# Kernel tuning notes

Measured on AMD Instinct MI355X. Metric: run time of the kernel, lower is better.

Reference implementation:

```python
import jax, jax.numpy as jnp
import numpy as np

B, T, D, E = 8, 4096, 128, 16
TOP_K = 2


def setup_inputs() -> dict:
    key = jax.random.key(0)
    k1, k2, k3 = jax.random.split(key, 3)
    x = jax.random.normal(k1, (B, T, D), dtype=jnp.float32)
    Wg = jax.random.normal(k2, (D, E), dtype=jnp.float32) * 0.08   # gate Dense kernel
    bg = jnp.zeros((E,), dtype=jnp.float32)                         # gate Dense bias
    Ew = jax.random.normal(k3, (E, D, D), dtype=jnp.float32) * (1.0 / np.sqrt(D))  # expert weights
    return {"x": x, "Wg": Wg, "bg": bg, "Ew": Ew}


def reference(x, Wg, bg, Ew):
    # gate: Dense(n_experts, softmax) on x (context defaults to x)
    gate_scores = jax.nn.softmax(x @ Wg + bg, axis=-1)              # (B,T,E)
    top_vals, top_idx = jax.lax.top_k(gate_scores, TOP_K)           # (B,T,2)
    top_w = top_vals / (jnp.sum(top_vals, axis=-1, keepdims=True) + 1e-6)
    # all-expert transform (faithful to original dense einsum)
    expert_outputs = jnp.einsum('btd,edo->bteo', x, Ew)             # (B,T,E,D)
    # combine top-k one-hot masks with normalized weights -> per-expert weight
    onehot = jax.nn.one_hot(top_idx, E, dtype=x.dtype)              # (B,T,2,E)
    mask = jnp.sum(onehot * top_w[..., None], axis=2)               # (B,T,E)
    m = mask[..., None]                                             # (B,T,E,1)
    weighted_avg = jnp.sum(expert_outputs * m, axis=2)              # (B,T,D)
    diff_sq = jnp.square(expert_outputs - weighted_avg[:, :, None, :])
    weighted_var = jnp.sum(diff_sq * m, axis=2)                     # (B,T,D)
    consensus = jnp.exp(-jnp.mean(weighted_var, axis=-1))           # (B,T)
    return (weighted_avg, consensus)
```

## Files before the change

kernel.cpp:

```cpp
#include <hip/hip_runtime.h>
#include <hip/hip_bf16.h>

#define NTOK 32768
#define DD 128
#define NE 16
#define CSTRIDE 32

#define OFF_COUNTS 0
#define OFF_TOKW   (4*1024)
#define OFF_LISTS  (512*1024)
#define OFF_YBUF   (4*1024*1024)

__global__ __launch_bounds__(128) void gate_kernel(
    const float* __restrict__ x, const float* __restrict__ Wg,
    const float* __restrict__ bg,
    int* __restrict__ counts, int* __restrict__ lists, float* __restrict__ tokw)
{
    __shared__ float sWg[DD * NE];
    __shared__ int   sCnt[NE];
    __shared__ int   sBase[NE];
    const int tid = threadIdx.x;
    for (int i = tid; i < DD * NE; i += 128) sWg[i] = Wg[i];
    if (tid < NE) sCnt[tid] = 0;
    __syncthreads();

    const int t = blockIdx.x * 128 + tid;
    const float* xt = x + (size_t)t * DD;

    float logits[NE];
    #pragma unroll
    for (int e = 0; e < NE; ++e) logits[e] = bg[e];

    #pragma unroll 4
    for (int d4 = 0; d4 < DD / 4; ++d4) {
        float4 xv = ((const float4*)xt)[d4];
        float xs0 = xv.x, xs1 = xv.y, xs2 = xv.z, xs3 = xv.w;
        const float* w0 = &sWg[(d4 * 4 + 0) * NE];
        const float* w1 = &sWg[(d4 * 4 + 1) * NE];
        const float* w2 = &sWg[(d4 * 4 + 2) * NE];
        const float* w3 = &sWg[(d4 * 4 + 3) * NE];
        #pragma unroll
        for (int e = 0; e < NE; ++e) {
            float acc = logits[e];
            acc = fmaf(xs0, w0[e], acc);
            acc = fmaf(xs1, w1[e], acc);
            acc = fmaf(xs2, w2[e], acc);
            acc = fmaf(xs3, w3[e], acc);
            logits[e] = acc;
        }
    }

    float m = logits[0];
    #pragma unroll
    for (int e = 1; e < NE; ++e) m = fmaxf(m, logits[e]);
    float Z = 0.0f;
    #pragma unroll
    for (int e = 0; e < NE; ++e) Z += expf(logits[e] - m);

    int i1 = 0; float l1 = logits[0];
    #pragma unroll
    for (int e = 1; e < NE; ++e) if (logits[e] > l1) { l1 = logits[e]; i1 = e; }
    int i2 = -1; float l2 = -3.4e38f;
    #pragma unroll
    for (int e = 0; e < NE; ++e) if (e != i1 && logits[e] > l2) { l2 = logits[e]; i2 = e; }

    float p1 = expf(l1 - m) / Z;
    float p2 = expf(l2 - m) / Z;
    float s  = p1 + p2 + 1e-6f;
    tokw[t * 2 + 0] = p1 / s;
    tokw[t * 2 + 1] = p2 / s;

    int s1 = atomicAdd(&sCnt[i1], 1);
    int s2 = atomicAdd(&sCnt[i2], 1);
    __syncthreads();
    if (tid < NE) sBase[tid] = atomicAdd(&counts[tid * CSTRIDE], sCnt[tid]);
    __syncthreads();
    lists[i1 * NTOK + sBase[i1] + s1] = t * 2 + 0;
    lists[i2 * NTOK + sBase[i2] + s2] = t * 2 + 1;
}

__global__ __launch_bounds__(256) void expert_kernel(
    const float* __restrict__ x, const float* __restrict__ Ew,
    const int* __restrict__ counts, const int* __restrict__ lists,
    float* __restrict__ ybuf)
{
    const int e = blockIdx.y;
    const int count = counts[e * CSTRIDE];
    const int start = blockIdx.x * 64;
    if (start >= count) return;

    __shared__ int   sEnt[64];
    __shared__ float xs[DD][64];
    __shared__ float ews[32][DD];

    const int tid = threadIdx.x;
    if (tid < 64) {
        int idx = start + tid;
        sEnt[tid] = (idx < count) ? lists[e * NTOK + idx] : -1;
    }
    __syncthreads();

    for (int i = tid; i < 64 * 32; i += 256) {
        int tok = i & 63, d4 = i >> 6;
        int en = sEnt[tok];
        if (en >= 0) {
            float4 v = ((const float4*)(x + (size_t)(en >> 1) * DD))[d4];
            xs[d4 * 4 + 0][tok] = v.x;
            xs[d4 * 4 + 1][tok] = v.y;
            xs[d4 * 4 + 2][tok] = v.z;
            xs[d4 * 4 + 3][tok] = v.w;
        }
    }

    const int lane = tid & 63, wv = tid >> 6;
    const int o4 = lane & 15, tq = lane >> 4;
    const int tokb = wv * 16 + tq * 4;
    const int colb = o4 * 4;

    float acc[4][8];
    #pragma unroll
    for (int a = 0; a < 4; ++a)
        #pragma unroll
        for (int b = 0; b < 8; ++b) acc[a][b] = 0.0f;

    const float* EwE = Ew + (size_t)e * DD * DD;

    for (int kt = 0; kt < 4; ++kt) {
        __syncthreads();
        for (int i = tid; i < 32 * 32; i += 256) {
            int row = i >> 5, c4 = i & 31;
            ((float4*)&ews[row][0])[c4] =
                ((const float4*)(EwE + (size_t)(kt * 32 + row) * DD))[c4];
        }
        __syncthreads();

        #pragma unroll 4
        for (int d = 0; d < 32; ++d) {
            float4 xv = *(const float4*)&xs[kt * 32 + d][tokb];
            float4 e0 = *(const float4*)&ews[d][colb];
            float4 e1 = *(const float4*)&ews[d][colb + 64];
            float xt0 = xv.x, xt1 = xv.y, xt2 = xv.z, xt3 = xv.w;
            acc[0][0] = fmaf(xt0, e0.x, acc[0][0]); acc[0][1] = fmaf(xt0, e0.y, acc[0][1]);
            acc[0][2] = fmaf(xt0, e0.z, acc[0][2]); acc[0][3] = fmaf(xt0, e0.w, acc[0][3]);
            acc[0][4] = fmaf(xt0, e1.x, acc[0][4]); acc[0][5] = fmaf(xt0, e1.y, acc[0][5]);
            acc[0][6] = fmaf(xt0, e1.z, acc[0][6]); acc[0][7] = fmaf(xt0, e1.w, acc[0][7]);
            acc[1][0] = fmaf(xt1, e0.x, acc[1][0]); acc[1][1] = fmaf(xt1, e0.y, acc[1][1]);
            acc[1][2] = fmaf(xt1, e0.z, acc[1][2]); acc[1][3] = fmaf(xt1, e0.w, acc[1][3]);
            acc[1][4] = fmaf(xt1, e1.x, acc[1][4]); acc[1][5] = fmaf(xt1, e1.y, acc[1][5]);
            acc[1][6] = fmaf(xt1, e1.z, acc[1][6]); acc[1][7] = fmaf(xt1, e1.w, acc[1][7]);
            acc[2][0] = fmaf(xt2, e0.x, acc[2][0]); acc[2][1] = fmaf(xt2, e0.y, acc[2][1]);
            acc[2][2] = fmaf(xt2, e0.z, acc[2][2]); acc[2][3] = fmaf(xt2, e0.w, acc[2][3]);
            acc[2][4] = fmaf(xt2, e1.x, acc[2][4]); acc[2][5] = fmaf(xt2, e1.y, acc[2][5]);
            acc[2][6] = fmaf(xt2, e1.z, acc[2][6]); acc[2][7] = fmaf(xt2, e1.w, acc[2][7]);
            acc[3][0] = fmaf(xt3, e0.x, acc[3][0]); acc[3][1] = fmaf(xt3, e0.y, acc[3][1]);
            acc[3][2] = fmaf(xt3, e0.z, acc[3][2]); acc[3][3] = fmaf(xt3, e0.w, acc[3][3]);
            acc[3][4] = fmaf(xt3, e1.x, acc[3][4]); acc[3][5] = fmaf(xt3, e1.y, acc[3][5]);
            acc[3][6] = fmaf(xt3, e1.z, acc[3][6]); acc[3][7] = fmaf(xt3, e1.w, acc[3][7]);
        }
    }

    #pragma unroll
    for (int tt = 0; tt < 4; ++tt) {
        int en = sEnt[tokb + tt];
        if (en >= 0) {
            float* yr = ybuf + (size_t)en * DD;
            float4 a; a.x = acc[tt][0]; a.y = acc[tt][1]; a.z = acc[tt][2]; a.w = acc[tt][3];
            float4 b; b.x = acc[tt][4]; b.y = acc[tt][5]; b.z = acc[tt][6]; b.w = acc[tt][7];
            *(float4*)(yr + colb)      = a;
            *(float4*)(yr + colb + 64) = b;
        }
    }
}

__global__ __launch_bounds__(256) void combine_kernel(
    const float* __restrict__ ybuf, const float* __restrict__ tokw,
    float* __restrict__ avg_out, float* __restrict__ cons_out)
{
    const int tid = threadIdx.x;
    const int lane = tid & 63, wv = tid >> 6;
    const int t = blockIdx.x * 4 + wv;

    const float w1 = tokw[t * 2 + 0];
    const float w2 = tokw[t * 2 + 1];
    const float2 y1 = ((const float2*)(ybuf + (size_t)(t * 2 + 0) * DD))[lane];
    const float2 y2 = ((const float2*)(ybuf + (size_t)(t * 2 + 1) * DD))[lane];

    float a0 = w1 * y1.x + w2 * y2.x;
    float a1 = w1 * y1.y + w2 * y2.y;
    float2 av; av.x = a0; av.y = a1;
    ((float2*)(avg_out + (size_t)t * DD))[lane] = av;

    float d10 = y1.x - a0, d11 = y1.y - a1;
    float d20 = y2.x - a0, d21 = y2.y - a1;
    float v = w1 * (d10 * d10 + d11 * d11) + w2 * (d20 * d20 + d21 * d21);
    #pragma unroll
    for (int off = 32; off > 0; off >>= 1) v += __shfl_xor(v, off);
    if (lane == 0) cons_out[t] = expf(-v * (1.0f / 128.0f));
}

extern "C" void kernel_launch(void* const* d_in, const int* in_sizes, int n_in,
                              void* d_out, int out_size, void* d_ws, size_t ws_size,
                              hipStream_t stream)
{
    const float* x  = (const float*)d_in[0];
    const float* Wg = (const float*)d_in[1];
    const float* bg = (const float*)d_in[2];
    const float* Ew = (const float*)d_in[3];
    float* out = (float*)d_out;

    char* ws = (char*)d_ws;
    int*   counts = (int*)(ws + OFF_COUNTS);
    float* tokw   = (float*)(ws + OFF_TOKW);
    int*   lists  = (int*)(ws + OFF_LISTS);
    float* ybuf   = (float*)(ws + OFF_YBUF);

    hipMemsetAsync(counts, 0, NE * CSTRIDE * sizeof(int), stream);

    gate_kernel<<<NTOK / 128, 128, 0, stream>>>(x, Wg, bg, counts, lists, tokw);
    expert_kernel<<<dim3(NTOK / 64, NE), 256, 0, stream>>>(x, Ew, counts, lists, ybuf);
    combine_kernel<<<NTOK / 4, 256, 0, stream>>>(ybuf, tokw, out, out + (size_t)NTOK * DD);
}
```

Baseline: 134.2 us.

## Use bf16 MFMA for expert matmul with pre-transposed bf16 weights and activations

Replaces the fp32 scalar-FMA expert GEMM with bf16 16x16x32 MFMA instructions. A new kernel converts expert weights to a transposed bf16 layout, and the gate kernel now also writes a bf16 copy of x. The gate splits each token's dot product across 4 lanes joined by shuffles. The expert output buffer is stored in bf16, halving the traffic into the combine kernel, which now handles 4 tokens per wave. Precision drops to bf16 for inputs and intermediates, which risks accuracy against the fp32 reference. The extra conversion kernel and the added xb write add some work in exchange.

After: 125.0 us. 1.07x faster.

```diff
diff --git a/kernel.cpp b/kernel.cpp
--- a/kernel.cpp
+++ b/kernel.cpp
@@ -9,45 +9,95 @@
 #define OFF_COUNTS 0
 #define OFF_TOKW   (4*1024)
 #define OFF_LISTS  (512*1024)
-#define OFF_YBUF   (4*1024*1024)
-
-__global__ __launch_bounds__(128) void gate_kernel(
+#define OFF_XB     (3*1024*1024)
+#define OFF_EWT    (11*1024*1024)
+#define OFF_YBUF   (12*1024*1024)
+
+typedef __attribute__((ext_vector_type(8))) short bf16x8;
+typedef __attribute__((ext_vector_type(4))) float f32x4;
+
+static __device__ inline ushort f2bf(float f) {
+    uint u = __builtin_bit_cast(uint, f);
+    u = u + 0x7FFFu + ((u >> 16) & 1u);
+    return (ushort)(u >> 16);
+}
+static __device__ inline float b2f(ushort h) {
+    uint u = ((uint)h) << 16;
+    return __builtin_bit_cast(float, u);
+}
+
+__global__ __launch_bounds__(256) void ewt_kernel(
+    const float* __restrict__ Ew, ushort* __restrict__ ewT)
+{
+    __shared__ float tile[32][33];
+    const int b = blockIdx.x;
+    const int e = b >> 4, ki = ((b >> 2) & 3) * 32, oi = (b & 3) * 32;
+    const int tid = threadIdx.x;
+    const int r = tid >> 3, c4 = (tid & 7) * 4;
+    const float4 v = *(const float4*)(Ew + (size_t)e * DD * DD + (ki + r) * DD + oi + c4);
+    tile[r][c4 + 0] = v.x; tile[r][c4 + 1] = v.y;
+    tile[r][c4 + 2] = v.z; tile[r][c4 + 3] = v.w;
+    __syncthreads();
+    const int o = tid >> 3, k4 = (tid & 7) * 4;
+    ushort4 s;
+    s.x = f2bf(tile[k4 + 0][o]);
+    s.y = f2bf(tile[k4 + 1][o]);
+    s.z = f2bf(tile[k4 + 2][o]);
+    s.w = f2bf(tile[k4 + 3][o]);
+    *(ushort4*)(ewT + (size_t)e * DD * DD + (oi + o) * DD + ki + k4) = s;
+}
+
+__global__ __launch_bounds__(256) void gate_kernel(
     const float* __restrict__ x, const float* __restrict__ Wg,
     const float* __restrict__ bg,
-    int* __restrict__ counts, int* __restrict__ lists, float* __restrict__ tokw)
+    int* __restrict__ counts, int* __restrict__ lists, float* __restrict__ tokw,
+    ushort* __restrict__ xb)
 {
     __shared__ float sWg[DD * NE];
+    __shared__ float sBg[NE];
     __shared__ int   sCnt[NE];
     __shared__ int   sBase[NE];
     const int tid = threadIdx.x;
-    for (int i = tid; i < DD * NE; i += 128) sWg[i] = Wg[i];
-    if (tid < NE) sCnt[tid] = 0;
-    __syncthreads();
-
-    const int t = blockIdx.x * 128 + tid;
+    for (int i = tid; i < DD * NE; i += 256) sWg[i] = Wg[i];
+    if (tid < NE) { sBg[tid] = bg[tid]; sCnt[tid] = 0; }
+    __syncthreads();
+
+    const int t = blockIdx.x * 64 + (tid >> 2);
+    const int g = tid & 3;
     const float* xt = x + (size_t)t * DD;
+    ushort*      xo = xb + (size_t)t * DD;
 
     float logits[NE];
     #pragma unroll
-    for (int e = 0; e < NE; ++e) logits[e] = bg[e];
-
-    #pragma unroll 4
-    for (int d4 = 0; d4 < DD / 4; ++d4) {
-        float4 xv = ((const float4*)xt)[d4];
-        float xs0 = xv.x, xs1 = xv.y, xs2 = xv.z, xs3 = xv.w;
-        const float* w0 = &sWg[(d4 * 4 + 0) * NE];
-        const float* w1 = &sWg[(d4 * 4 + 1) * NE];
-        const float* w2 = &sWg[(d4 * 4 + 2) * NE];
-        const float* w3 = &sWg[(d4 * 4 + 3) * NE];
+    for (int e = 0; e < NE; ++e) logits[e] = 0.0f;
+
+    #pragma unroll
+    for (int i = 0; i < 8; ++i) {
+        const int d0 = g * 4 + i * 16;
+        float4 v = ((const float4*)xt)[g + i * 4];
+        const float* w0 = &sWg[(d0 + 0) * NE];
+        const float* w1 = &sWg[(d0 + 1) * NE];
+        const float* w2 = &sWg[(d0 + 2) * NE];
+        const float* w3 = &sWg[(d0 + 3) * NE];
         #pragma unroll
         for (int e = 0; e < NE; ++e) {
-            float acc = logits[e];
-            acc = fmaf(xs0, w0[e], acc);
-            acc = fmaf(xs1, w1[e], acc);
-            acc = fmaf(xs2, w2[e], acc);
-            acc = fmaf(xs3, w3[e], acc);
-            logits[e] = acc;
-        }
+            float a = logits[e];
+            a = fmaf(v.x, w0[e], a);
+            a = fmaf(v.y, w1[e], a);
+            a = fmaf(v.z, w2[e], a);
+            a = fmaf(v.w, w3[e], a);
+            logits[e] = a;
+        }
+        ushort4 s; s.x = f2bf(v.x); s.y = f2bf(v.y); s.z = f2bf(v.z); s.w = f2bf(v.w);
+        *(ushort4*)(xo + d0) = s;
+    }
+
+    #pragma unroll
+    for (int e = 0; e < NE; ++e) {
+        float a = logits[e];
+        a += __shfl_xor(a, 1);
+        a += __shfl_xor(a, 2);
+        logits[e] = a + sBg[e];
     }
 
     float m = logits[0];
@@ -64,138 +114,119 @@
     #pragma unroll
     for (int e = 0; e < NE; ++e) if (e != i1 && logits[e] > l2) { l2 = logits[e]; i2 = e; }
 
-    float p1 = expf(l1 - m) / Z;
-    float p2 = expf(l2 - m) / Z;
-    float s  = p1 + p2 + 1e-6f;
-    tokw[t * 2 + 0] = p1 / s;
-    tokw[t * 2 + 1] = p2 / s;
-
-    int s1 = atomicAdd(&sCnt[i1], 1);
-    int s2 = atomicAdd(&sCnt[i2], 1);
+    int s1 = 0, s2 = 0;
+    if (g == 0) {
+        float p1 = expf(l1 - m) / Z;
+        float p2 = expf(l2 - m) / Z;
+        float s  = p1 + p2 + 1e-6f;
+        tokw[t * 2 + 0] = p1 / s;
+        tokw[t * 2 + 1] = p2 / s;
+        s1 = atomicAdd(&sCnt[i1], 1);
+        s2 = atomicAdd(&sCnt[i2], 1);
+    }
     __syncthreads();
     if (tid < NE) sBase[tid] = atomicAdd(&counts[tid * CSTRIDE], sCnt[tid]);
     __syncthreads();
-    lists[i1 * NTOK + sBase[i1] + s1] = t * 2 + 0;
-    lists[i2 * NTOK + sBase[i2] + s2] = t * 2 + 1;
+    if (g == 0) {
+        lists[i1 * NTOK + sBase[i1] + s1] = t * 2 + 0;
+        lists[i2 * NTOK + sBase[i2] + s2] = t * 2 + 1;
+    }
 }
 
 __global__ __launch_bounds__(256) void expert_kernel(
-    const float* __restrict__ x, const float* __restrict__ Ew,
+    const ushort* __restrict__ xb, const ushort* __restrict__ ewT,
     const int* __restrict__ counts, const int* __restrict__ lists,
-    float* __restrict__ ybuf)
+    ushort* __restrict__ ybuf)
 {
     const int e = blockIdx.y;
     const int count = counts[e * CSTRIDE];
     const int start = blockIdx.x * 64;
     if (start >= count) return;
 
-    __shared__ int   sEnt[64];
-    __shared__ float xs[DD][64];
-    __shared__ float ews[32][DD];
-
-    const int tid = threadIdx.x;
-    if (tid < 64) {
-        int idx = start + tid;
-        sEnt[tid] = (idx < count) ? lists[e * NTOK + idx] : -1;
-    }
-    __syncthreads();
-
-    for (int i = tid; i < 64 * 32; i += 256) {
-        int tok = i & 63, d4 = i >> 6;
-        int en = sEnt[tok];
-        if (en >= 0) {
-            float4 v = ((const float4*)(x + (size_t)(en >> 1) * DD))[d4];
-            xs[d4 * 4 + 0][tok] = v.x;
-            xs[d4 * 4 + 1][tok] = v.y;
-            xs[d4 * 4 + 2][tok] = v.z;
-            xs[d4 * 4 + 3][tok] = v.w;
-        }
-    }
-
+    const int tid  = threadIdx.x;
     const int lane = tid & 63, wv = tid >> 6;
-    const int o4 = lane & 15, tq = lane >> 4;
-    const int tokb = wv * 16 + tq * 4;
-    const int colb = o4 * 4;
-
-    float acc[4][8];
-    #pragma unroll
-    for (int a = 0; a < 4; ++a)
+    const int row  = lane & 15;
+    const int kg   = lane >> 4;
+
+    const int idx = start + wv * 16 + row;
+    const int en  = (idx < count) ? lists[e * NTOK + idx] : -1;
+    const ushort* xrow = xb + (size_t)((en < 0 ? 0 : en) >> 1) * DD;
+
+    bf16x8 xf[4];
+    #pragma unroll
+    for (int k = 0; k < 4; ++k)
+        xf[k] = *(const bf16x8*)(xrow + k * 32 + kg * 8);
+
+    const ushort* ewe = ewT + (size_t)e * DD * DD;
+    f32x4 acc[8];
+    #pragma unroll
+    for (int n = 0; n < 8; ++n) acc[n] = (f32x4)(0.0f);
+
+    #pragma unroll
+    for (int n = 0; n < 8; ++n) {
+        const ushort* er = ewe + (size_t)(n * 16 + row) * DD + kg * 8;
         #pragma unroll
-        for (int b = 0; b < 8; ++b) acc[a][b] = 0.0f;
-
-    const float* EwE = Ew + (size_t)e * DD * DD;
-
-    for (int kt = 0; kt < 4; ++kt) {
-        __syncthreads();
-        for (int i = tid; i < 32 * 32; i += 256) {
-            int row = i >> 5, c4 = i & 31;
-            ((float4*)&ews[row][0])[c4] =
-                ((const float4*)(EwE + (size_t)(kt * 32 + row) * DD))[c4];
-        }
-        __syncthreads();
-
-        #pragma unroll 4
-        for (int d = 0; d < 32; ++d) {
-            float4 xv = *(const float4*)&xs[kt * 32 + d][tokb];
-            float4 e0 = *(const float4*)&ews[d][colb];
-            float4 e1 = *(const float4*)&ews[d][colb + 64];
-            float xt0 = xv.x, xt1 = xv.y, xt2 = xv.z, xt3 = xv.w;
-            acc[0][0] = fmaf(xt0, e0.x, acc[0][0]); acc[0][1] = fmaf(xt0, e0.y, acc[0][1]);
-            acc[0][2] = fmaf(xt0, e0.z, acc[0][2]); acc[0][3] = fmaf(xt0, e0.w, acc[0][3]);
-            acc[0][4] = fmaf(xt0, e1.x, acc[0][4]); acc[0][5] = fmaf(xt0, e1.y, acc[0][5]);
-            acc[0][6] = fmaf(xt0, e1.z, acc[0][6]); acc[0][7] = fmaf(xt0, e1.w, acc[0][7]);
-            acc[1][0] = fmaf(xt1, e0.x, acc[1][0]); acc[1][1] = fmaf(xt1, e0.y, acc[1][1]);
-            acc[1][2] = fmaf(xt1, e0.z, acc[1][2]); acc[1][3] = fmaf(xt1, e0.w, acc[1][3]);
-            acc[1][4] = fmaf(xt1, e1.x, acc[1][4]); acc[1][5] = fmaf(xt1, e1.y, acc[1][5]);
-            acc[1][6] = fmaf(xt1, e1.z, acc[1][6]); acc[1][7] = fmaf(xt1, e1.w, acc[1][7]);
-            acc[2][0] = fmaf(xt2, e0.x, acc[2][0]); acc[2][1] = fmaf(xt2, e0.y, acc[2][1]);
-            acc[2][2] = fmaf(xt2, e0.z, acc[2][2]); acc[2][3] = fmaf(xt2, e0.w, acc[2][3]);
-            acc[2][4] = fmaf(xt2, e1.x, acc[2][4]); acc[2][5] = fmaf(xt2, e1.y, acc[2][5]);
-            acc[2][6] = fmaf(xt2, e1.z, acc[2][6]); acc[2][7] = fmaf(xt2, e1.w, acc[2][7]);
-            acc[3][0] = fmaf(xt3, e0.x, acc[3][0]); acc[3][1] = fmaf(xt3, e0.y, acc[3][1]);
-            acc[3][2] = fmaf(xt3, e0.z, acc[3][2]); acc[3][3] = fmaf(xt3, e0.w, acc[3][3]);
-            acc[3][4] = fmaf(xt3, e1.x, acc[3][4]); acc[3][5] = fmaf(xt3, e1.y, acc[3][5]);
-            acc[3][6] = fmaf(xt3, e1.z, acc[3][6]); acc[3][7] = fmaf(xt3, e1.w, acc[3][7]);
-        }
-    }
-
-    #pragma unroll
-    for (int tt = 0; tt < 4; ++tt) {
-        int en = sEnt[tokb + tt];
-        if (en >= 0) {
-            float* yr = ybuf + (size_t)en * DD;
-            float4 a; a.x = acc[tt][0]; a.y = acc[tt][1]; a.z = acc[tt][2]; a.w = acc[tt][3];
-            float4 b; b.x = acc[tt][4]; b.y = acc[tt][5]; b.z = acc[tt][6]; b.w = acc[tt][7];
-            *(float4*)(yr + colb)      = a;
-            *(float4*)(yr + colb + 64) = b;
+        for (int k = 0; k < 4; ++k) {
+            bf16x8 ef = *(const bf16x8*)(er + k * 32);
+            acc[n] = __builtin_amdgcn_mfma_f32_16x16x32_bf16(ef, xf[k], acc[n], 0, 0, 0);
+        }
+    }
+
+    if (en >= 0) {
+        ushort* yr = ybuf + (size_t)en * DD + kg * 4;
+        #pragma unroll
+        for (int n = 0; n < 8; ++n) {
+            ushort4 s;
+            s.x = f2bf(acc[n][0]); s.y = f2bf(acc[n][1]);
+            s.z = f2bf(acc[n][2]); s.w = f2bf(acc[n][3]);
+            *(ushort4*)(yr + n * 16) = s;
         }
     }
 }
 
 __global__ __launch_bounds__(256) void combine_kernel(
-    const float* __restrict__ ybuf, const float* __restrict__ tokw,
+    const ushort* __restrict__ ybuf, const float* __restrict__ tokw,
     float* __restrict__ avg_out, float* __restrict__ cons_out)
 {
     const int tid = threadIdx.x;
     const int lane = tid & 63, wv = tid >> 6;
-    const int t = blockIdx.x * 4 + wv;
-
-    const float w1 = tokw[t * 2 + 0];
-    const float w2 = tokw[t * 2 + 1];
-    const float2 y1 = ((const float2*)(ybuf + (size_t)(t * 2 + 0) * DD))[lane];
-    const float2 y2 = ((const float2*)(ybuf + (size_t)(t * 2 + 1) * DD))[lane];
-
-    float a0 = w1 * y1.x + w2 * y2.x;
-    float a1 = w1 * y1.y + w2 * y2.y;
-    float2 av; av.x = a0; av.y = a1;
-    ((float2*)(avg_out + (size_t)t * DD))[lane] = av;
-
-    float d10 = y1.x - a0, d11 = y1.y - a1;
-    float d20 = y2.x - a0, d21 = y2.y - a1;
-    float v = w1 * (d10 * d10 + d11 * d11) + w2 * (d20 * d20 + d21 * d21);
-    #pragma unroll
-    for (int off = 32; off > 0; off >>= 1) v += __shfl_xor(v, off);
-    if (lane == 0) cons_out[t] = expf(-v * (1.0f / 128.0f));
+    const int half = lane >> 5, hl = lane & 31;
+    const int t0 = blockIdx.x * 16 + wv * 4;
+
+    #pragma unroll
+    for (int j = 0; j < 4; ++j) {
+        const int t = t0 + j;
+        const float w1 = tokw[t * 2 + 0];
+        const float w2 = tokw[t * 2 + 1];
+        const float wo = half ? w2 : w1;
+        const float wx = half ? w1 : w2;
+
+        ushort4 raw = *(const ushort4*)(ybuf + (size_t)(t * 2 + half) * DD + hl * 4);
+        float o0 = b2f(raw.x), o1 = b2f(raw.y), o2 = b2f(raw.z), o3 = b2f(raw.w);
+        float x0 = __shfl_xor(o0, 32);
+        float x1 = __shfl_xor(o1, 32);
+        float x2 = __shfl_xor(o2, 32);
+        float x3 = __shfl_xor(o3, 32);
+
+        float a0 = wo * o0 + wx * x0;
+        float a1 = wo * o1 + wx * x1;
+        float a2 = wo * o2 + wx * x2;
+        float a3 = wo * o3 + wx * x3;
+        if (half == 0) {
+            float4 av; av.x = a0; av.y = a1; av.z = a2; av.w = a3;
+            ((float4*)(avg_out + (size_t)t * DD))[hl] = av;
+        }
+        float d0 = o0 - a0, d1 = o1 - a1, d2 = o2 - a2, d3 = o3 - a3;
+        float e0 = x0 - a0, e1 = x1 - a1, e2 = x2 - a2, e3 = x3 - a3;
+        float v = wo * (d0*d0 + d1*d1 + d2*d2 + d3*d3)
+                + wx * (e0*e0 + e1*e1 + e2*e2 + e3*e3);
+        v += __shfl_xor(v, 1);
+        v += __shfl_xor(v, 2);
+        v += __shfl_xor(v, 4);
+        v += __shfl_xor(v, 8);
+        v += __shfl_xor(v, 16);
+        if (lane == 0) cons_out[t] = expf(-v * (1.0f / 128.0f));
+    }
 }
 
 extern "C" void kernel_launch(void* const* d_in, const int* in_sizes, int n_in,
@@ -209,14 +240,17 @@
     float* out = (float*)d_out;
 
     char* ws = (char*)d_ws;
-    int*   counts = (int*)(ws + OFF_COUNTS);
-    float* tokw   = (float*)(ws + OFF_TOKW);
-    int*   lists  = (int*)(ws + OFF_LISTS);
-    float* ybuf   = (float*)(ws + OFF_YBUF);
+    int*    counts = (int*)(ws + OFF_COUNTS);
+    float*  tokw   = (float*)(ws + OFF_TOKW);
+    int*    lists  = (int*)(ws + OFF_LISTS);
+    ushort* xbuf   = (ushort*)(ws + OFF_XB);
+    ushort* ewT    = (ushort*)(ws + OFF_EWT);
+    ushort* ybuf   = (ushort*)(ws + OFF_YBUF);
 
     hipMemsetAsync(counts, 0, NE * CSTRIDE * sizeof(int), stream);
 
-    gate_kernel<<<NTOK / 128, 128, 0, stream>>>(x, Wg, bg, counts, lists, tokw);
-    expert_kernel<<<dim3(NTOK / 64, NE), 256, 0, stream>>>(x, Ew, counts, lists, ybuf);
-    combine_kernel<<<NTOK / 4, 256, 0, stream>>>(ybuf, tokw, out, out + (size_t)NTOK * DD);
-}
+    ewt_kernel<<<256, 256, 0, stream>>>(Ew, ewT);
+    gate_kernel<<<NTOK / 64, 256, 0, stream>>>(x, Wg, bg, counts, lists, tokw, xbuf);
+    expert_kernel<<<dim3(NTOK / 64, NE), 256, 0, stream>>>(xbuf, ewT, counts, lists, ybuf);
+    combine_kernel<<<NTOK / 16, 256, 0, stream>>>(ybuf, tokw, out, out + (size_t)NTOK * DD);
+}
```
